# Performance work log

Measured on AMD Instinct MI355X. Metric: run time of the kernel, lower is better.

## Reference

```python
import jax, jax.numpy as jnp
import numpy as np

N_NODES = 100000
N_EDGES = 1600000
IN_DIM = 128
OUT_DIM = 64


def setup_inputs() -> dict:
    key = jax.random.key(0)
    k = jax.random.split(key, 6)
    h = jax.random.normal(k[0], (N_NODES, IN_DIM), dtype=jnp.float32)
    W_fc = jax.random.normal(k[1], (IN_DIM, OUT_DIM), dtype=jnp.float32) / np.float32(np.sqrt(IN_DIM))
    W_attn = jax.random.normal(k[2], (2 * OUT_DIM, 1), dtype=jnp.float32) / np.float32(np.sqrt(2 * OUT_DIM))
    W_edge = jax.random.normal(k[3], (2 * OUT_DIM, OUT_DIM), dtype=jnp.float32) / np.float32(np.sqrt(2 * OUT_DIM))
    src = jax.random.randint(k[4], (N_EDGES,), 0, N_NODES, dtype=jnp.int32)
    dst = jax.random.randint(k[5], (N_EDGES,), 0, N_NODES, dtype=jnp.int32)
    return {"h": h, "W_fc": W_fc, "W_attn": W_attn, "W_edge": W_edge, "src": src, "dst": dst}


def reference(h, W_fc, W_attn, W_edge, src, dst):
    # node projection: z = fc(h)
    z = h @ W_fc                                   # [N, out_dim]
    # gather per-edge src/dst features and concat (edge_type == 0 branch)
    z2 = jnp.concatenate([z[src], z[dst]], axis=1)  # [E, 2*out_dim]
    a = (z2 @ W_attn)[:, 0]                         # [E] attention logits
    e = z2 @ W_edge                                 # [E, out_dim] edge messages
    # segment softmax over incoming edges of each destination node
    a_max = jax.ops.segment_max(a, dst, num_segments=N_NODES)   # [N]
    w = jnp.exp(a - a_max[dst])                                  # [E]
    denom = jax.ops.segment_sum(w, dst, num_segments=N_NODES)    # [N]
    alpha = w / denom[dst]                                       # [E]
    # weighted scatter-add of neighbor features + sum of edge messages
    h1 = jax.ops.segment_sum(alpha[:, None] * z[src], dst, num_segments=N_NODES)
    h2 = jax.ops.segment_sum(e, dst, num_segments=N_NODES)
    return h1 + h2
```

## Files before the change

### kernel.cpp

```cpp
#include <hip/hip_runtime.h>

#define IN_DIM 128
#define OUT_DIM 64

#define NB 256
#define BSHIFT 9
#define NPB 512
#define EPT 16

typedef __attribute__((ext_vector_type(8))) short short8;
typedef __attribute__((ext_vector_type(4))) float f32x4;

__device__ __forceinline__ unsigned pack_bf16x2(float a, float b) {
    unsigned ua = __float_as_uint(a), ub = __float_as_uint(b);
    ua = (ua + 0x7fffu + ((ua >> 16) & 1u)) >> 16;
    ub = (ub + 0x7fffu + ((ub >> 16) & 1u)) >> 16;
    return ua | (ub << 16);
}

__global__ void precompute_weights(const float* __restrict__ W_fc,
                                   const float* __restrict__ W_edge,
                                   float* __restrict__ W1, float* __restrict__ W2) {
    int k = blockIdx.x;
    int j = threadIdx.x;
    __shared__ float row[64];
    row[j] = W_fc[k * 64 + j];
    __syncthreads();
    float s1 = 0.f, s2 = 0.f;
    #pragma unroll 8
    for (int m = 0; m < 64; ++m) {
        float w = row[m];
        s1 = fmaf(w, W_edge[m * 64 + j], s1);
        s2 = fmaf(w, W_edge[(64 + m) * 64 + j], s2);
    }
    W1[k * 64 + j] = s1;
    W2[k * 64 + j] = s2;
}

__global__ void pack_bfrags(const float* __restrict__ W_fc, const float* __restrict__ W1,
                            const float* __restrict__ W2, unsigned* __restrict__ bfrag) {
    int slot = blockIdx.x * 256 + threadIdx.x;
    if (slot >= 12 * 4 * 64) return;
    int lane = slot & 63;
    int ks = (slot >> 6) & 3;
    int t = slot >> 8;
    int grp = t >> 2;
    int col = (t & 3) * 16 + (lane & 15);
    int kbase = ks * 32 + (lane >> 4) * 8;
    const float* W = (grp == 0) ? W_fc : ((grp == 1) ? W1 : W2);
    unsigned o0 = pack_bf16x2(W[(kbase + 0) * 64 + col], W[(kbase + 1) * 64 + col]);
    unsigned o1 = pack_bf16x2(W[(kbase + 2) * 64 + col], W[(kbase + 3) * 64 + col]);
    unsigned o2 = pack_bf16x2(W[(kbase + 4) * 64 + col], W[(kbase + 5) * 64 + col]);
    unsigned o3 = pack_bf16x2(W[(kbase + 6) * 64 + col], W[(kbase + 7) * 64 + col]);
    ((uint4*)bfrag)[slot] = make_uint4(o0, o1, o2, o3);
}

__global__ __launch_bounds__(256) void node_gemm(
    const float* __restrict__ h, const unsigned* __restrict__ bfrag,
    const float* __restrict__ W_attn,
    unsigned* __restrict__ zes, float* __restrict__ ed,
    float* __restrict__ ws_, int N)
{
    __shared__ uint4 lds4[1024];
    char* lds = (char*)lds4;
    const int tid = threadIdx.x;
    const int lane = tid & 63;
    const int w = tid >> 6;
    const int n0 = blockIdx.x * 64;

    #pragma unroll
    for (int r = 0; r < 8; ++r) {
        int idx = r * 256 + tid;
        int row = idx >> 5;
        int c4 = idx & 31;
        float4 v = make_float4(0.f, 0.f, 0.f, 0.f);
        int n = n0 + row;
        if (n < N) v = *(const float4*)(h + (size_t)n * IN_DIM + c4 * 4);
        int byte = (row << 8) + (c4 << 3);
        byte ^= ((row & 7) << 4);
        *(uint2*)(lds + byte) = make_uint2(pack_bf16x2(v.x, v.y), pack_bf16x2(v.z, v.w));
    }
    __syncthreads();

    const int g = lane >> 4;
    const int c = lane & 15;

    union U { uint4 u; short8 s; };
    U a[4];
    {
        const int arow = (w << 4) + c;
        #pragma unroll
        for (int ks = 0; ks < 4; ++ks) {
            int byte = (arow << 8) + (ks << 6) + (g << 4);
            byte ^= ((arow & 7) << 4);
            a[ks].u = *(const uint4*)(lds + byte);
        }
    }

    f32x4 acc[12];
    #pragma unroll
    for (int t = 0; t < 12; ++t) acc[t] = (f32x4){0.f, 0.f, 0.f, 0.f};

    const uint4* bf4 = (const uint4*)bfrag;
    #pragma unroll
    for (int t = 0; t < 12; ++t) {
        #pragma unroll
        for (int ks = 0; ks < 4; ++ks) {
            U b; b.u = bf4[(t * 4 + ks) * 64 + lane];
            acc[t] = __builtin_amdgcn_mfma_f32_16x16x32_bf16(a[ks].s, b.s, acc[t], 0, 0, 0);
        }
    }

    const float wa0 = W_attn[c], wa1 = W_attn[16 + c], wa2 = W_attn[32 + c], wa3 = W_attn[48 + c];
    #pragma unroll
    for (int r = 0; r < 4; ++r) {
        const int n = n0 + (w << 4) + (g << 2) + r;
        float part = acc[0][r] * wa0 + acc[1][r] * wa1 + acc[2][r] * wa2 + acc[3][r] * wa3;
        part += __shfl_xor(part, 1);
        part += __shfl_xor(part, 2);
        part += __shfl_xor(part, 4);
        part += __shfl_xor(part, 8);
        if (n < N) {
            #pragma unroll
            for (int t = 0; t < 4; ++t) {
                const int col = t * 16 + c;
                zes[(size_t)n * 64 + col] = pack_bf16x2(acc[t][r], acc[t + 4][r]);
                ed [(size_t)n * 64 + col] = acc[t + 8][r];
            }
            if (c == 0) ws_[n] = expf(part);
        }
    }
}

__global__ __launch_bounds__(256) void coarse_hist(const int* __restrict__ dst,
                                                   unsigned* __restrict__ hist, int E) {
    __shared__ unsigned hl[NB];
    const int t = threadIdx.x;
    hl[t] = 0;
    __syncthreads();
    const int base = blockIdx.x * (256 * EPT);
    const int lim = min(base + 256 * EPT, E);
    for (int i = base + t; i < lim; i += 256)
        atomicAdd(&hl[((unsigned)dst[i]) >> BSHIFT], 1u);
    __syncthreads();
    if (hl[t]) atomicAdd(&hist[t], hl[t]);
}

__global__ void bucket_scan(const unsigned* __restrict__ hist,
                            unsigned* __restrict__ bucketBase, unsigned* __restrict__ cursor) {
    __shared__ unsigned s[NB];
    const int t = threadIdx.x;
    unsigned v = hist[t];
    s[t] = v; __syncthreads();
    for (int off = 1; off < NB; off <<= 1) {
        unsigned add = (t >= off) ? s[t - off] : 0u;
        __syncthreads();
        s[t] += add;
        __syncthreads();
    }
    unsigned excl = s[t] - v;
    bucketBase[t] = excl;
    cursor[t] = excl;
    if (t == NB - 1) bucketBase[NB] = s[t];
}

__global__ __launch_bounds__(256) void coarse_scatter(
    const int* __restrict__ src, const int* __restrict__ dst,
    unsigned* __restrict__ cursor, uint2* __restrict__ pairs, int E)
{
    __shared__ unsigned h[NB];
    __shared__ unsigned start[NB];
    const int t = threadIdx.x;
    h[t] = 0;
    __syncthreads();
    const int base = blockIdx.x * (256 * EPT);
    unsigned sv[EPT], dv[EPT], rk[EPT];
    #pragma unroll
    for (int k = 0; k < EPT; ++k) {
        int i = base + k * 256 + t;
        bool valid = i < E;
        unsigned s = 0, d = 0;
        if (valid) { s = (unsigned)src[i]; d = (unsigned)dst[i]; }
        sv[k] = s;
        dv[k] = valid ? d : 0xFFFFFFFFu;
        rk[k] = valid ? atomicAdd(&h[d >> BSHIFT], 1u) : 0u;
    }
    __syncthreads();
    start[t] = h[t] ? atomicAdd(&cursor[t], h[t]) : 0u;
    __syncthreads();
    #pragma unroll
    for (int k = 0; k < EPT; ++k) {
        if (dv[k] != 0xFFFFFFFFu) {
            unsigned b = dv[k] >> BSHIFT;
            pairs[start[b] + rk[k]] = make_uint2(sv[k], dv[k] & (NPB - 1));
        }
    }
}

__global__ __launch_bounds__(256) void fine_bin(
    const uint2* __restrict__ pairs, const unsigned* __restrict__ bucketBase,
    unsigned* __restrict__ offs, int* __restrict__ src_sorted, int N, int E)
{
    __shared__ unsigned deg[NPB];
    __shared__ unsigned excl[NPB];
    __shared__ unsigned pscan[256];
    const int b = blockIdx.x;
    const int t = threadIdx.x;
    const int node0 = b << BSHIFT;
    const unsigned e0 = bucketBase[b], e1 = bucketBase[b + 1];

    deg[t] = 0; deg[t + 256] = 0;
    __syncthreads();
    for (unsigned i = e0 + t; i < e1; i += 256)
        atomicAdd(&deg[pairs[i].y], 1u);
    __syncthreads();

    unsigned a0 = deg[2 * t], a1 = deg[2 * t + 1];
    unsigned ps = a0 + a1;
    pscan[t] = ps;
    __syncthreads();
    for (int off = 1; off < 256; off <<= 1) {
        unsigned add = (t >= off) ? pscan[t - off] : 0u;
        __syncthreads();
        pscan[t] += add;
        __syncthreads();
    }
    unsigned exclP = pscan[t] - ps;
    excl[2 * t] = exclP;
    excl[2 * t + 1] = exclP + a0;
    __syncthreads();

    #pragma unroll
    for (int l = t; l < NPB; l += 256) {
        int n = node0 + l;
        if (n < N) offs[n] = e0 + excl[l];
    }
    if (b == 0 && t == 0) offs[N] = (unsigned)E;
    __syncthreads();

    for (unsigned i = e0 + t; i < e1; i += 256) {
        uint2 p = pairs[i];
        unsigned pos = e0 + atomicAdd(&excl[p.y], 1u);
        src_sorted[pos] = (int)p.x;
    }
}

__global__ __launch_bounds__(256) void gather_nodes(
    const int* __restrict__ src_sorted, const unsigned* __restrict__ offs,
    const float* __restrict__ ws_, const unsigned* __restrict__ zes,
    const float* __restrict__ ed, float* __restrict__ out, int N)
{
    const int lane = threadIdx.x & 63;
    const int g = lane >> 4;
    const int c4 = lane & 15;
    const int d = blockIdx.x * 4 + (threadIdx.x >> 6);
    if (d >= N) return;
    const unsigned o0 = offs[d], o1 = offs[d + 1];
    const int deg = (int)(o1 - o0);

    float az0 = 0.f, az1 = 0.f, az2 = 0.f, az3 = 0.f;
    float ae0 = 0.f, ae1 = 0.f, ae2 = 0.f, ae3 = 0.f;
    float lsum = 0.f;

    for (unsigned o = o0; o < o1; o += 64) {
        const int rem = min(64, (int)(o1 - o));
        int s = 0; float w = 0.f;
        if (lane < rem) { s = src_sorted[o + lane]; w = ws_[s]; }
        lsum += w;
        for (int j = 0; j < rem; j += 4) {
            int s0 = __builtin_amdgcn_readlane(s, j);
            int s1 = __builtin_amdgcn_readlane(s, j + 1);
            int s2 = __builtin_amdgcn_readlane(s, j + 2);
            int s3 = __builtin_amdgcn_readlane(s, j + 3);
            float w0 = __uint_as_float(__builtin_amdgcn_readlane(__float_as_uint(w), j));
            float w1 = __uint_as_float(__builtin_amdgcn_readlane(__float_as_uint(w), j + 1));
            float w2 = __uint_as_float(__builtin_amdgcn_readlane(__float_as_uint(w), j + 2));
            float w3 = __uint_as_float(__builtin_amdgcn_readlane(__float_as_uint(w), j + 3));
            int   sg = (g == 0) ? s0 : ((g == 1) ? s1 : ((g == 2) ? s2 : s3));
            float wg = (g == 0) ? w0 : ((g == 1) ? w1 : ((g == 2) ? w2 : w3));
            const bool valid = (j + g) < rem;
            const uint4 u = *(const uint4*)&zes[(size_t)sg * 64 + c4 * 4];
            float z0 = __uint_as_float(u.x << 16), e0 = __uint_as_float(u.x & 0xffff0000u);
            float z1 = __uint_as_float(u.y << 16), e1 = __uint_as_float(u.y & 0xffff0000u);
            float z2 = __uint_as_float(u.z << 16), e2 = __uint_as_float(u.z & 0xffff0000u);
            float z3 = __uint_as_float(u.w << 16), e3 = __uint_as_float(u.w & 0xffff0000u);
            az0 = fmaf(wg, z0, az0); ae0 += valid ? e0 : 0.f;
            az1 = fmaf(wg, z1, az1); ae1 += valid ? e1 : 0.f;
            az2 = fmaf(wg, z2, az2); ae2 += valid ? e2 : 0.f;
            az3 = fmaf(wg, z3, az3); ae3 += valid ? e3 : 0.f;
        }
    }

    az0 += __shfl_xor(az0, 16); az0 += __shfl_xor(az0, 32);
    az1 += __shfl_xor(az1, 16); az1 += __shfl_xor(az1, 32);
    az2 += __shfl_xor(az2, 16); az2 += __shfl_xor(az2, 32);
    az3 += __shfl_xor(az3, 16); az3 += __shfl_xor(az3, 32);
    ae0 += __shfl_xor(ae0, 16); ae0 += __shfl_xor(ae0, 32);
    ae1 += __shfl_xor(ae1, 16); ae1 += __shfl_xor(ae1, 32);
    ae2 += __shfl_xor(ae2, 16); ae2 += __shfl_xor(ae2, 32);
    ae3 += __shfl_xor(ae3, 16); ae3 += __shfl_xor(ae3, 32);
    #pragma unroll
    for (int off = 32; off; off >>= 1) lsum += __shfl_xor(lsum, off);

    if (g == 0) {
        const float inv = (lsum > 0.f) ? 1.f / lsum : 0.f;
        const float4 edv = *(const float4*)&ed[(size_t)d * 64 + c4 * 4];
        float4 r;
        r.x = fmaf((float)deg, edv.x, fmaf(az0, inv, ae0));
        r.y = fmaf((float)deg, edv.y, fmaf(az1, inv, ae1));
        r.z = fmaf((float)deg, edv.z, fmaf(az2, inv, ae2));
        r.w = fmaf((float)deg, edv.w, fmaf(az3, inv, ae3));
        *(float4*)&out[(size_t)d * 64 + c4 * 4] = r;
    }
}

extern "C" void kernel_launch(void* const* d_in, const int* in_sizes, int n_in,
                              void* d_out, int out_size, void* d_ws, size_t ws_size,
                              hipStream_t stream) {
    const float* h      = (const float*)d_in[0];
    const float* W_fc   = (const float*)d_in[1];
    const float* W_attn = (const float*)d_in[2];
    const float* W_edge = (const float*)d_in[3];
    const int*   src    = (const int*)d_in[4];
    const int*   dst    = (const int*)d_in[5];
    float* out = (float*)d_out;

    const int N = in_sizes[0] / IN_DIM;
    const int E = in_sizes[4];

    char* p = (char*)d_ws;
    auto alloc = [&](size_t bytes) -> void* {
        void* r = (void*)p;
        p += (bytes + 255) & ~(size_t)255;
        return r;
    };
    unsigned* zes    = (unsigned*)alloc((size_t)N * 64 * 4);
    float*    ed     = (float*)alloc((size_t)N * 64 * 4);
    float*    ws_    = (float*)alloc((size_t)N * 4);
    unsigned* offs   = (unsigned*)alloc((size_t)(N + 1) * 4);
    unsigned* hist   = (unsigned*)alloc(NB * 4);
    unsigned* bbase  = (unsigned*)alloc((NB + 1) * 4);
    unsigned* cursor = (unsigned*)alloc(NB * 4);
    uint2*    pairs  = (uint2*)alloc((size_t)E * 8);
    int*      src_s  = (int*)alloc((size_t)E * 4);
    float*    W1     = (float*)alloc(128 * 64 * 4);
    float*    W2     = (float*)alloc(128 * 64 * 4);
    unsigned* bfrag  = (unsigned*)alloc((size_t)12 * 4 * 64 * 16);

    hipMemsetAsync(hist, 0, NB * 4, stream);

    precompute_weights<<<128, 64, 0, stream>>>(W_fc, W_edge, W1, W2);
    pack_bfrags<<<12, 256, 0, stream>>>(W_fc, W1, W2, bfrag);

    int blocksA = (N + 63) / 64;
    node_gemm<<<blocksA, 256, 0, stream>>>(h, bfrag, W_attn, zes, ed, ws_, N);

    int blocksC = (E + 256 * EPT - 1) / (256 * EPT);
    coarse_hist<<<blocksC, 256, 0, stream>>>(dst, hist, E);
    bucket_scan<<<1, NB, 0, stream>>>(hist, bbase, cursor);
    coarse_scatter<<<blocksC, 256, 0, stream>>>(src, dst, cursor, pairs, E);
    fine_bin<<<NB, 256, 0, stream>>>(pairs, bbase, offs, src_s, N, E);

    gather_nodes<<<(N + 3) / 4, 256, 0, stream>>>(src_s, offs, ws_, zes, ed, out, N);
}
```

Measured before the change: 253.7 us.

## Pack binning pairs to 32-bit, pre-scale source offsets, use bpermute in gather

Coarse scatter now packs each edge's source id and local destination index into a single 32-bit word, halving pair traffic through scatter and fine binning. Fine binning stores pre-shifted byte offsets of source rows, so the gather kernel can address zes directly. The gather broadcasts offset and weight with ds_bpermute instead of four readlanes plus selects. It also drops the per-edge valid mask by pointing inactive lanes at a padding row N, which node_gemm now writes. This relies on row N being zero, i.e. out-of-range h rows in node_gemm being zero-filled, and on the src<<9 packing fitting in 32 bits.

```diff
diff --git a/kernel.cpp b/kernel.cpp
--- a/kernel.cpp
+++ b/kernel.cpp
@@ -120,7 +120,7 @@
         part += __shfl_xor(part, 2);
         part += __shfl_xor(part, 4);
         part += __shfl_xor(part, 8);
-        if (n < N) {
+        if (n <= N) {
             #pragma unroll
             for (int t = 0; t < 4; ++t) {
                 const int col = t * 16 + c;
@@ -166,7 +166,7 @@
 
 __global__ __launch_bounds__(256) void coarse_scatter(
     const int* __restrict__ src, const int* __restrict__ dst,
-    unsigned* __restrict__ cursor, uint2* __restrict__ pairs, int E)
+    unsigned* __restrict__ cursor, unsigned* __restrict__ pairs, int E)
 {
     __shared__ unsigned h[NB];
     __shared__ unsigned start[NB];
@@ -174,15 +174,15 @@
     h[t] = 0;
     __syncthreads();
     const int base = blockIdx.x * (256 * EPT);
-    unsigned sv[EPT], dv[EPT], rk[EPT];
+    unsigned pv[EPT], bk[EPT], rk[EPT];
     #pragma unroll
     for (int k = 0; k < EPT; ++k) {
         int i = base + k * 256 + t;
         bool valid = i < E;
         unsigned s = 0, d = 0;
         if (valid) { s = (unsigned)src[i]; d = (unsigned)dst[i]; }
-        sv[k] = s;
-        dv[k] = valid ? d : 0xFFFFFFFFu;
+        pv[k] = (s << BSHIFT) | (d & (NPB - 1));
+        bk[k] = valid ? (d >> BSHIFT) : 0xFFFFFFFFu;
         rk[k] = valid ? atomicAdd(&h[d >> BSHIFT], 1u) : 0u;
     }
     __syncthreads();
@@ -190,16 +190,14 @@
     __syncthreads();
     #pragma unroll
     for (int k = 0; k < EPT; ++k) {
-        if (dv[k] != 0xFFFFFFFFu) {
-            unsigned b = dv[k] >> BSHIFT;
-            pairs[start[b] + rk[k]] = make_uint2(sv[k], dv[k] & (NPB - 1));
-        }
+        if (bk[k] != 0xFFFFFFFFu)
+            pairs[start[bk[k]] + rk[k]] = pv[k];
     }
 }
 
 __global__ __launch_bounds__(256) void fine_bin(
-    const uint2* __restrict__ pairs, const unsigned* __restrict__ bucketBase,
-    unsigned* __restrict__ offs, int* __restrict__ src_sorted, int N, int E)
+    const unsigned* __restrict__ pairs, const unsigned* __restrict__ bucketBase,
+    unsigned* __restrict__ offs, int* __restrict__ srcoff_sorted, int N, int E)
 {
     __shared__ unsigned deg[NPB];
     __shared__ unsigned excl[NPB];
@@ -212,7 +210,7 @@
     deg[t] = 0; deg[t + 256] = 0;
     __syncthreads();
     for (unsigned i = e0 + t; i < e1; i += 256)
-        atomicAdd(&deg[pairs[i].y], 1u);
+        atomicAdd(&deg[pairs[i] & (NPB - 1)], 1u);
     __syncthreads();
 
     unsigned a0 = deg[2 * t], a1 = deg[2 * t + 1];
@@ -239,24 +237,27 @@
     __syncthreads();
 
     for (unsigned i = e0 + t; i < e1; i += 256) {
-        uint2 p = pairs[i];
-        unsigned pos = e0 + atomicAdd(&excl[p.y], 1u);
-        src_sorted[pos] = (int)p.x;
+        unsigned p = pairs[i];
+        unsigned loc = p & (NPB - 1);
+        unsigned pos = e0 + atomicAdd(&excl[loc], 1u);
+        srcoff_sorted[pos] = (int)((p >> BSHIFT) << 8);
     }
 }
 
 __global__ __launch_bounds__(256) void gather_nodes(
-    const int* __restrict__ src_sorted, const unsigned* __restrict__ offs,
+    const int* __restrict__ srcoff_sorted, const unsigned* __restrict__ offs,
     const float* __restrict__ ws_, const unsigned* __restrict__ zes,
     const float* __restrict__ ed, float* __restrict__ out, int N)
 {
     const int lane = threadIdx.x & 63;
-    const int g = lane >> 4;
-    const int c4 = lane & 15;
+    const int goff4 = (lane >> 4) << 2;
+    const int c4off = (lane & 15) << 4;
     const int d = blockIdx.x * 4 + (threadIdx.x >> 6);
     if (d >= N) return;
     const unsigned o0 = offs[d], o1 = offs[d + 1];
     const int deg = (int)(o1 - o0);
+    const int zoff = N << 8;
+    const char* zesb = (const char*)zes;
 
     float az0 = 0.f, az1 = 0.f, az2 = 0.f, az3 = 0.f;
     float ae0 = 0.f, ae1 = 0.f, ae2 = 0.f, ae3 = 0.f;
@@ -264,30 +265,19 @@
 
     for (unsigned o = o0; o < o1; o += 64) {
         const int rem = min(64, (int)(o1 - o));
-        int s = 0; float w = 0.f;
-        if (lane < rem) { s = src_sorted[o + lane]; w = ws_[s]; }
+        int soff = zoff; float w = 0.f;
+        if (lane < rem) { soff = srcoff_sorted[o + lane]; w = ws_[(unsigned)soff >> 8]; }
         lsum += w;
         for (int j = 0; j < rem; j += 4) {
-            int s0 = __builtin_amdgcn_readlane(s, j);
-            int s1 = __builtin_amdgcn_readlane(s, j + 1);
-            int s2 = __builtin_amdgcn_readlane(s, j + 2);
-            int s3 = __builtin_amdgcn_readlane(s, j + 3);
-            float w0 = __uint_as_float(__builtin_amdgcn_readlane(__float_as_uint(w), j));
-            float w1 = __uint_as_float(__builtin_amdgcn_readlane(__float_as_uint(w), j + 1));
-            float w2 = __uint_as_float(__builtin_amdgcn_readlane(__float_as_uint(w), j + 2));
-            float w3 = __uint_as_float(__builtin_amdgcn_readlane(__float_as_uint(w), j + 3));
-            int   sg = (g == 0) ? s0 : ((g == 1) ? s1 : ((g == 2) ? s2 : s3));
-            float wg = (g == 0) ? w0 : ((g == 1) ? w1 : ((g == 2) ? w2 : w3));
-            const bool valid = (j + g) < rem;
-            const uint4 u = *(const uint4*)&zes[(size_t)sg * 64 + c4 * 4];
-            float z0 = __uint_as_float(u.x << 16), e0 = __uint_as_float(u.x & 0xffff0000u);
-            float z1 = __uint_as_float(u.y << 16), e1 = __uint_as_float(u.y & 0xffff0000u);
-            float z2 = __uint_as_float(u.z << 16), e2 = __uint_as_float(u.z & 0xffff0000u);
-            float z3 = __uint_as_float(u.w << 16), e3 = __uint_as_float(u.w & 0xffff0000u);
-            az0 = fmaf(wg, z0, az0); ae0 += valid ? e0 : 0.f;
-            az1 = fmaf(wg, z1, az1); ae1 += valid ? e1 : 0.f;
-            az2 = fmaf(wg, z2, az2); ae2 += valid ? e2 : 0.f;
-            az3 = fmaf(wg, z3, az3); ae3 += valid ? e3 : 0.f;
+            const int idx4 = (j << 2) + goff4;
+            const int so = __builtin_amdgcn_ds_bpermute(idx4, soff);
+            const float wg = __uint_as_float(
+                (unsigned)__builtin_amdgcn_ds_bpermute(idx4, (int)__float_as_uint(w)));
+            const uint4 u = *(const uint4*)(zesb + (unsigned)(so + c4off));
+            az0 = fmaf(wg, __uint_as_float(u.x << 16), az0); ae0 += __uint_as_float(u.x & 0xffff0000u);
+            az1 = fmaf(wg, __uint_as_float(u.y << 16), az1); ae1 += __uint_as_float(u.y & 0xffff0000u);
+            az2 = fmaf(wg, __uint_as_float(u.z << 16), az2); ae2 += __uint_as_float(u.z & 0xffff0000u);
+            az3 = fmaf(wg, __uint_as_float(u.w << 16), az3); ae3 += __uint_as_float(u.w & 0xffff0000u);
         }
     }
 
@@ -302,15 +292,15 @@
     #pragma unroll
     for (int off = 32; off; off >>= 1) lsum += __shfl_xor(lsum, off);
 
-    if (g == 0) {
+    if (goff4 == 0) {
         const float inv = (lsum > 0.f) ? 1.f / lsum : 0.f;
-        const float4 edv = *(const float4*)&ed[(size_t)d * 64 + c4 * 4];
+        const float4 edv = *(const float4*)&ed[(size_t)d * 64 + (c4off >> 2)];
         float4 r;
         r.x = fmaf((float)deg, edv.x, fmaf(az0, inv, ae0));
         r.y = fmaf((float)deg, edv.y, fmaf(az1, inv, ae1));
         r.z = fmaf((float)deg, edv.z, fmaf(az2, inv, ae2));
         r.w = fmaf((float)deg, edv.w, fmaf(az3, inv, ae3));
-        *(float4*)&out[(size_t)d * 64 + c4 * 4] = r;
+        *(float4*)&out[(size_t)d * 64 + (c4off >> 2)] = r;
     }
 }
 
@@ -334,14 +324,14 @@
         p += (bytes + 255) & ~(size_t)255;
         return r;
     };
-    unsigned* zes    = (unsigned*)alloc((size_t)N * 64 * 4);
-    float*    ed     = (float*)alloc((size_t)N * 64 * 4);
-    float*    ws_    = (float*)alloc((size_t)N * 4);
+    unsigned* zes    = (unsigned*)alloc((size_t)(N + 1) * 64 * 4);
+    float*    ed     = (float*)alloc((size_t)(N + 1) * 64 * 4);
+    float*    ws_    = (float*)alloc((size_t)(N + 1) * 4);
     unsigned* offs   = (unsigned*)alloc((size_t)(N + 1) * 4);
     unsigned* hist   = (unsigned*)alloc(NB * 4);
     unsigned* bbase  = (unsigned*)alloc((NB + 1) * 4);
     unsigned* cursor = (unsigned*)alloc(NB * 4);
-    uint2*    pairs  = (uint2*)alloc((size_t)E * 8);
+    unsigned* pairs  = (unsigned*)alloc((size_t)E * 4);
     int*      src_s  = (int*)alloc((size_t)E * 4);
     float*    W1     = (float*)alloc(128 * 64 * 4);
     float*    W2     = (float*)alloc(128 * 64 * 4);
```

Result: no change. 257.7 us (+1.6%).
